# Performance work log

Measured on AMD Instinct MI355X. Metric: run time of the kernel, lower is better.

Reference implementation:

```python
import jax, jax.numpy as jnp
import numpy as np
from math import sqrt

KERNEL = 25
INV_SQRT2 = 1.0 / sqrt(2.0)


def _moving_avg(xt):
    # xt: [B, L]; replicate-pad then average-pool k=25 stride=1 -> [B, L]
    pad_l = (KERNEL - 1) // 2
    pad_r = KERNEL - 1 - pad_l
    xp = jnp.pad(xt, ((0, 0), (pad_l, pad_r)), mode='edge')[:, None, :]  # [B,1,Lp]
    k = jnp.full((1, 1, KERNEL), 1.0 / KERNEL, dtype=xt.dtype)  # [O,I,W]
    out = jax.lax.conv_general_dilated(xp, k, window_strides=(1,), padding='VALID',
                                       dimension_numbers=('NCH', 'OIH', 'NCH'))
    return out[:, 0, :]


def setup_inputs() -> dict:
    key = jax.random.key(0)
    ks = jax.random.split(key, 7)
    B, L, P, H = 8192, 4096, 720, 2048
    return {
        'x': jax.random.normal(ks[0], (B, L, 1), dtype=jnp.float32),
        'W_trend': jax.random.normal(ks[1], (P, L), dtype=jnp.float32) * 0.02,
        'b_trend': jax.random.normal(ks[2], (P,), dtype=jnp.float32) * 0.02,
        'W_lo': jax.random.normal(ks[3], (P, H), dtype=jnp.float32) * 0.02,
        'b_lo': jax.random.normal(ks[4], (P,), dtype=jnp.float32) * 0.02,
        'W_hi': jax.random.normal(ks[5], (P, H), dtype=jnp.float32) * 0.02,
        'b_hi': jax.random.normal(ks[6], (P,), dtype=jnp.float32) * 0.02,
    }


def reference(x, W_trend, b_trend, W_lo, b_lo, W_hi, b_hi):
    xt = x[..., 0]                              # [B, L]
    trend = _moving_avg(xt)                     # [B, L]
    res = xt - trend                            # [B, L]
    res_mean = jnp.mean(res, axis=-1, keepdims=True)
    # torch.std is unbiased (ddof=1)
    res_std = jnp.std(res, axis=-1, keepdims=True, ddof=1) + 1e-5
    res_norm = (res - res_mean) / res_std       # [B, L]
    # Haar DWT (stride-2 conv with [1,1]/sqrt2 and [1,-1]/sqrt2); L even -> no pad
    even, odd = res_norm[:, 0::2], res_norm[:, 1::2]  # [B, L/2]
    res_lo = (even + odd) * INV_SQRT2
    res_hi = (even - odd) * INV_SQRT2
    pred_trend = trend @ W_trend.T + b_trend    # [B, P]
    pred_res = (res_lo @ W_lo.T + b_lo) + (res_hi @ W_hi.T + b_hi)
    total = pred_trend + pred_res * res_std     # res_std broadcasts [B,1]
    return total[..., None]                     # [B, P, 1]
```

## Files before the change

kernel.cpp:

```cpp
#include <hip/hip_runtime.h>

typedef unsigned short u16;
typedef unsigned int   u32;
typedef __attribute__((ext_vector_type(8))) short bf16x8;
typedef __attribute__((ext_vector_type(4))) float f32x4;

#define LROW 4096
#define NB   8192
#define PCOL 720
#define NPAD 768
#define HH   2048
#define INV_SQRT2F 0.70710678118654752440f

#define WS_XBF_BYTES ((size_t)67108864)
#define WS_G_BYTES   ((size_t)6291456)
#define WS_MIN       (WS_XBF_BYTES + WS_G_BYTES + (size_t)NB * 4)

__device__ __forceinline__ u16 f2bf(float f) {
    union { float f; u32 u; } v; v.f = f;
    u32 r = v.u + 0x7FFFu + ((v.u >> 16) & 1u);
    return (u16)(r >> 16);
}

#define SWZ(i) ((i) ^ (((i) >> 5) & 31))

__global__ __launch_bounds__(256) void prep_rows(const float* __restrict__ x,
                                                 u16* __restrict__ xbf,
                                                 float* __restrict__ stdv) {
    __shared__ float S[LROW];
    __shared__ float wred[4];
    __shared__ float ends[2];
    __shared__ float rred[8];
    const int tid = threadIdx.x;
    const int lane = tid & 63, wv = tid >> 6;
    const size_t b = blockIdx.x;

    const float4* xr4 = (const float4*)(x + b * LROW);
    float4 q0 = xr4[tid * 4 + 0], q1 = xr4[tid * 4 + 1];
    float4 q2 = xr4[tid * 4 + 2], q3 = xr4[tid * 4 + 3];
    float r[16];
    r[0]=q0.x; r[1]=q0.y; r[2]=q0.z; r[3]=q0.w;
    r[4]=q1.x; r[5]=q1.y; r[6]=q1.z; r[7]=q1.w;
    r[8]=q2.x; r[9]=q2.y; r[10]=q2.z; r[11]=q2.w;
    r[12]=q3.x; r[13]=q3.y; r[14]=q3.z; r[15]=q3.w;

    float ps[16];
    float a = 0.f;
    #pragma unroll
    for (int k = 0; k < 16; ++k) { a += r[k]; ps[k] = a; }
    const float segsum = a;

    float v = segsum;
    #pragma unroll
    for (int off = 1; off < 64; off <<= 1) {
        float o = __shfl_up(v, off);
        if (lane >= off) v += o;
    }
    if (lane == 63) wred[wv] = v;
    if (tid == 0)   ends[0] = r[0];
    if (tid == 255) ends[1] = r[15];
    __syncthreads();

    float wbase = 0.f;
    #pragma unroll
    for (int w = 0; w < 4; ++w) if (w < wv) wbase += wred[w];
    const float ebase = wbase + v - segsum;

    #pragma unroll
    for (int k = 0; k < 16; ++k) {
        const int i = (tid << 4) + k;
        S[SWZ(i)] = ebase + ps[k];
    }
    __syncthreads();

    const float x0 = ends[0], xl = ends[1];
    float s1 = 0.f, s2 = 0.f;
    u16 ob[16];
    #pragma unroll
    for (int k = 0; k < 16; ++k) {
        const int i = (tid << 4) + k;
        int h = i + 12; h = h > LROW - 1 ? LROW - 1 : h;
        float wsum = S[SWZ(h)];
        if (i >= 13) wsum -= S[SWZ(i - 13)];
        if (i < 12) wsum += (float)(12 - i) * x0;
        if (i > LROW - 13) wsum += (float)(i - (LROW - 13)) * xl;
        const float xi = r[k];
        const float rr = xi - wsum * 0.04f;
        s1 += rr; s2 += rr * rr;
        ob[k] = f2bf(xi);
    }

    uint4 o0, o1;
    o0.x = (u32)ob[0]  | ((u32)ob[1]  << 16);
    o0.y = (u32)ob[2]  | ((u32)ob[3]  << 16);
    o0.z = (u32)ob[4]  | ((u32)ob[5]  << 16);
    o0.w = (u32)ob[6]  | ((u32)ob[7]  << 16);
    o1.x = (u32)ob[8]  | ((u32)ob[9]  << 16);
    o1.y = (u32)ob[10] | ((u32)ob[11] << 16);
    o1.z = (u32)ob[12] | ((u32)ob[13] << 16);
    o1.w = (u32)ob[14] | ((u32)ob[15] << 16);
    uint4* op = (uint4*)(xbf + b * LROW + ((size_t)tid << 4));
    op[0] = o0; op[1] = o1;

    #pragma unroll
    for (int off = 32; off; off >>= 1) {
        s1 += __shfl_down(s1, off);
        s2 += __shfl_down(s2, off);
    }
    if (lane == 0) { rred[wv * 2] = s1; rred[wv * 2 + 1] = s2; }
    __syncthreads();
    if (tid == 0) {
        const float S1 = rred[0] + rred[2] + rred[4] + rred[6];
        const float S2 = rred[1] + rred[3] + rred[5] + rred[7];
        const float mean = S1 / (float)LROW;
        float var = (S2 - (float)LROW * mean * mean) / (float)(LROW - 1);
        var = var < 0.f ? 0.f : var;
        stdv[b] = sqrtf(var) + 1e-5f;
    }
}

__global__ __launch_bounds__(256) void prep_weights(const float* __restrict__ Wt,
                                                    const float* __restrict__ Wlo,
                                                    const float* __restrict__ Whi,
                                                    u16* __restrict__ Gm) {
    __shared__ float S[LROW];
    __shared__ float wred[4];
    __shared__ float sred[4];
    const int tid = threadIdx.x;
    const int lane = tid & 63, wv = tid >> 6;
    const int p = blockIdx.x;
    u16* grow = Gm + (size_t)p * LROW;
    if (p >= PCOL) {
        uint4 z; z.x = z.y = z.z = z.w = 0u;
        uint4* g4 = (uint4*)grow;
        for (int i = tid; i < LROW / 8; i += 256) g4[i] = z;
        return;
    }
    const float4* wt4 = (const float4*)(Wt + (size_t)p * LROW);
    float4 q0 = wt4[tid * 4 + 0], q1 = wt4[tid * 4 + 1];
    float4 q2 = wt4[tid * 4 + 2], q3 = wt4[tid * 4 + 3];
    const float4* lo4 = (const float4*)(Wlo + (size_t)p * HH);
    const float4* hi4 = (const float4*)(Whi + (size_t)p * HH);
    float4 a0 = lo4[tid * 2 + 0], a1 = lo4[tid * 2 + 1];
    float4 b0 = hi4[tid * 2 + 0], b1 = hi4[tid * 2 + 1];

    float w[16];
    w[0]=q0.x; w[1]=q0.y; w[2]=q0.z; w[3]=q0.w;
    w[4]=q1.x; w[5]=q1.y; w[6]=q1.z; w[7]=q1.w;
    w[8]=q2.x; w[9]=q2.y; w[10]=q2.z; w[11]=q2.w;
    w[12]=q3.x; w[13]=q3.y; w[14]=q3.z; w[15]=q3.w;
    float lv[8] = {a0.x,a0.y,a0.z,a0.w,a1.x,a1.y,a1.z,a1.w};
    float hv[8] = {b0.x,b0.y,b0.z,b0.w,b1.x,b1.y,b1.z,b1.w};

    float u[16], z_[16];
    float slo = 0.f;
    #pragma unroll
    for (int j = 0; j < 8; ++j) {
        u[2*j]   = (lv[j] + hv[j]) * INV_SQRT2F;
        u[2*j+1] = (lv[j] - hv[j]) * INV_SQRT2F;
        slo += lv[j];
    }
    #pragma unroll
    for (int k = 0; k < 16; ++k) z_[k] = w[k] - u[k];

    float ps[16];
    float a = 0.f;
    #pragma unroll
    for (int k = 0; k < 16; ++k) { a += z_[k]; ps[k] = a; }
    const float segsum = a;

    float v = segsum;
    #pragma unroll
    for (int off = 1; off < 64; off <<= 1) {
        float o = __shfl_up(v, off);
        if (lane >= off) v += o;
    }
    if (lane == 63) wred[wv] = v;
    #pragma unroll
    for (int off = 32; off; off >>= 1) slo += __shfl_down(slo, off);
    if (lane == 0) sred[wv] = slo;
    __syncthreads();

    float wbase = 0.f;
    #pragma unroll
    for (int ww = 0; ww < 4; ++ww) if (ww < wv) wbase += wred[ww];
    const float ebase = wbase + v - segsum;
    const float SLO = sred[0] + sred[1] + sred[2] + sred[3];

    #pragma unroll
    for (int k = 0; k < 16; ++k) {
        const int i = (tid << 4) + k;
        S[SWZ(i)] = ebase + ps[k];
    }
    __syncthreads();

    const float coef = -1.4142135623730951f * SLO / (float)LROW;
    u16 ob[16];
    #pragma unroll
    for (int k = 0; k < 16; ++k) {
        const int l = (tid << 4) + k;
        float zT;
        if (l == 0) {
            float acc = 0.f;
            for (int m = 0; m <= 12; ++m) acc += S[SWZ(m)];
            zT = acc * 0.04f;
        } else if (l == LROW - 1) {
            float acc = 0.f;
            for (int m = 0; m <= 12; ++m) acc += S[SWZ(LROW - 2 - m)];
            zT = (13.f * S[SWZ(LROW - 1)] - acc) * 0.04f;
        } else {
            int h = l + 12; h = h > LROW - 1 ? LROW - 1 : h;
            float t_ = S[SWZ(h)];
            if (l >= 13) t_ -= S[SWZ(l - 13)];
            zT = t_ * 0.04f;
        }
        float c;
        const int dmin = l < (LROW - 1 - l) ? l : (LROW - 1 - l);
        if (dmin >= 12)      c = 0.f;
        else if (dmin == 0)  c = -66.f / 25.f;
        else                 c = (float)(12 - dmin) * 0.04f;
        ob[k] = f2bf(zT + u[k] + coef * c);
    }

    uint4 o0, o1;
    o0.x = (u32)ob[0]  | ((u32)ob[1]  << 16);
    o0.y = (u32)ob[2]  | ((u32)ob[3]  << 16);
    o0.z = (u32)ob[4]  | ((u32)ob[5]  << 16);
    o0.w = (u32)ob[6]  | ((u32)ob[7]  << 16);
    o1.x = (u32)ob[8]  | ((u32)ob[9]  << 16);
    o1.y = (u32)ob[10] | ((u32)ob[11] << 16);
    o1.z = (u32)ob[12] | ((u32)ob[13] << 16);
    o1.w = (u32)ob[14] | ((u32)ob[15] << 16);
    uint4* op = (uint4*)(grow + ((size_t)tid << 4));
    op[0] = o0; op[1] = o1;
}

typedef __attribute__((address_space(1))) void gvoid;
typedef __attribute__((address_space(3))) void lvoid;
__device__ __forceinline__ void gld16(const void* g, void* l) {
    __builtin_amdgcn_global_load_lds((gvoid*)g, (lvoid*)l, 16, 0, 0);
}

#define TILE_B   14336
#define NTILES   128

#define WAITVM(a, b) do { \
    if (wid < 2) asm volatile("s_waitcnt vmcnt(" #a ")" ::: "memory"); \
    else         asm volatile("s_waitcnt vmcnt(" #b ")" ::: "memory"); \
} while (0)

#define STAGE(T) do { \
    char* sb_ = smb + ((T) & 3) * TILE_B; \
    const size_t go_ = (size_t)(T) * 64; \
    gld16(g0 + go_, sb_ + lo0); \
    gld16(g1 + go_, sb_ + lo1); \
    gld16(g2 + go_, sb_ + lo2); \
    if (wid < 2) gld16(g3 + go_, sb_ + lo3); \
} while (0)

#define BODY(T, VMA, VMB, DOSTAGE) do { \
    WAITVM(VMA, VMB); \
    __builtin_amdgcn_s_barrier(); \
    __builtin_amdgcn_sched_barrier(0); \
    const char* sa_ = smb + ((T) & 3) * TILE_B; \
    bf16x8 af0 = *(const bf16x8*)(sa_ + aoff); \
    bf16x8 af1 = *(const bf16x8*)(sa_ + aoff + 1024); \
    bf16x8 af2 = *(const bf16x8*)(sa_ + aoff + 2048); \
    bf16x8 af3 = *(const bf16x8*)(sa_ + aoff + 3072); \
    bf16x8 bv0 = *(const bf16x8*)(sa_ + boff); \
    bf16x8 bv1 = *(const bf16x8*)(sa_ + boff + 1024); \
    bf16x8 bv2 = *(const bf16x8*)(sa_ + boff + 2048); \
    if (DOSTAGE) STAGE((T) + 3); \
    asm volatile("s_waitcnt lgkmcnt(0)" ::: "memory"); \
    __builtin_amdgcn_sched_barrier(0); \
    __builtin_amdgcn_s_setprio(1); \
    acc[0][0] = __builtin_amdgcn_mfma_f32_16x16x32_bf16(af0, bv0, acc[0][0], 0, 0, 0); \
    acc[0][1] = __builtin_amdgcn_mfma_f32_16x16x32_bf16(af0, bv1, acc[0][1], 0, 0, 0); \
    acc[0][2] = __builtin_amdgcn_mfma_f32_16x16x32_bf16(af0, bv2, acc[0][2], 0, 0, 0); \
    acc[1][0] = __builtin_amdgcn_mfma_f32_16x16x32_bf16(af1, bv0, acc[1][0], 0, 0, 0); \
    acc[1][1] = __builtin_amdgcn_mfma_f32_16x16x32_bf16(af1, bv1, acc[1][1], 0, 0, 0); \
    acc[1][2] = __builtin_amdgcn_mfma_f32_16x16x32_bf16(af1, bv2, acc[1][2], 0, 0, 0); \
    acc[2][0] = __builtin_amdgcn_mfma_f32_16x16x32_bf16(af2, bv0, acc[2][0], 0, 0, 0); \
    acc[2][1] = __builtin_amdgcn_mfma_f32_16x16x32_bf16(af2, bv1, acc[2][1], 0, 0, 0); \
    acc[2][2] = __builtin_amdgcn_mfma_f32_16x16x32_bf16(af2, bv2, acc[2][2], 0, 0, 0); \
    acc[3][0] = __builtin_amdgcn_mfma_f32_16x16x32_bf16(af3, bv0, acc[3][0], 0, 0, 0); \
    acc[3][1] = __builtin_amdgcn_mfma_f32_16x16x32_bf16(af3, bv1, acc[3][1], 0, 0, 0); \
    acc[3][2] = __builtin_amdgcn_mfma_f32_16x16x32_bf16(af3, bv2, acc[3][2], 0, 0, 0); \
    __builtin_amdgcn_s_setprio(0); \
} while (0)

__global__ __launch_bounds__(256, 2) void gemm_fused(const u16* __restrict__ Abf,
                                                     const u16* __restrict__ Gbf,
                                                     const float* __restrict__ bt,
                                                     const float* __restrict__ bl,
                                                     const float* __restrict__ bh,
                                                     const float* __restrict__ stdv,
                                                     float* __restrict__ out) {
    __shared__ __align__(16) char Sm[4 * TILE_B];
    char* smb = (char*)Sm;
    const int tid = threadIdx.x;
    const int l = tid & 63, wid = tid >> 6;

    const int orig = blockIdx.x;
    const int chunk = orig & 7, pos = orig >> 3;
    const int bx = pos & 7;
    const int by = (chunk << 3) + (pos >> 3);
    const int m0 = by * 128;
    const int n0 = bx * 96;

    const int sgb = (((l & 3) ^ ((l >> 3) & 3)) << 4);
    const int rsub = l >> 2;
    const char* gmat = (wid < 2) ? (const char*)Abf : (const char*)Gbf;
    const int row00 = (wid < 2) ? (m0 + wid * 64) : (n0 + (wid - 2) * 48);
    const int lob   = (wid < 2) ? (wid * 4096) : (8192 + (wid - 2) * 3072);
    const char* g0 = gmat + (((size_t)(row00 +  0 + rsub)) << 13) + sgb;
    const char* g1 = gmat + (((size_t)(row00 + 16 + rsub)) << 13) + sgb;
    const char* g2 = gmat + (((size_t)(row00 + 32 + rsub)) << 13) + sgb;
    const char* g3 = gmat + (((size_t)(row00 + 48 + rsub)) << 13) + sgb;
    const int lo0 = lob, lo1 = lob + 1024, lo2 = lob + 2048, lo3 = lob + 3072;

    const int wm = wid >> 1, wn = wid & 1;
    const int soff = (((l >> 4) ^ ((l >> 1) & 3)) << 4);
    const int aoff = (wm * 64 + (l & 15)) * 64 + soff;
    const int boff = 8192 + (wn * 48 + (l & 15)) * 64 + soff;

    f32x4 acc[4][3] = {};

    STAGE(0); STAGE(1); STAGE(2);

    for (int t = 0; t < NTILES - 3; ++t) {
        BODY(t, 8, 6, 1);
    }
    BODY(NTILES - 3, 8, 6, 0);
    BODY(NTILES - 2, 4, 3, 0);
    BODY(NTILES - 1, 0, 0, 0);

    const int crow = m0 + wm * 64 + ((l >> 4) << 2);
    const int ccol = n0 + wn * 48 + (l & 15);
    float btv[3], bsv[3];
    #pragma unroll
    for (int n = 0; n < 3; ++n) {
        const int col = ccol + n * 16;
        if (col < PCOL) { btv[n] = bt[col]; bsv[n] = bl[col] + bh[col]; }
        else            { btv[n] = 0.f; bsv[n] = 0.f; }
    }
    #pragma unroll
    for (int m = 0; m < 4; ++m) {
        const int row = crow + m * 16;
        const float4 sv = *(const float4*)(stdv + row);
        #pragma unroll
        for (int n = 0; n < 3; ++n) {
            const int col = ccol + n * 16;
            if (col < PCOL) {
                float* orow = out + (size_t)row * PCOL + col;
                #pragma unroll
                for (int j = 0; j < 4; ++j) {
                    const float s = (j == 0) ? sv.x : (j == 1) ? sv.y : (j == 2) ? sv.z : sv.w;
                    orow[(size_t)j * PCOL] = acc[m][n][j] + btv[n] + s * bsv[n];
                }
            }
        }
    }
}

extern "C" void kernel_launch(void* const* d_in, const int* in_sizes, int n_in,
                              void* d_out, int out_size, void* d_ws, size_t ws_size,
                              hipStream_t stream) {
    (void)in_sizes; (void)n_in; (void)out_size;
    if (ws_size < WS_MIN) return;

    const float* x  = (const float*)d_in[0];
    const float* Wt = (const float*)d_in[1];
    const float* bt = (const float*)d_in[2];
    const float* Wl = (const float*)d_in[3];
    const float* bl = (const float*)d_in[4];
    const float* Wh = (const float*)d_in[5];
    const float* bh = (const float*)d_in[6];
    float* out = (float*)d_out;

    char* ws = (char*)d_ws;
    u16*   xbf = (u16*)ws;
    u16*   Gm  = (u16*)(ws + WS_XBF_BYTES);
    float* sd  = (float*)(ws + WS_XBF_BYTES + WS_G_BYTES);

    prep_rows<<<NB, 256, 0, stream>>>(x, xbf, sd);
    prep_weights<<<NPAD, 256, 0, stream>>>(Wt, Wl, Wh, Gm);
    gemm_fused<<<512, 256, 0, stream>>>(xbf, Gm, bt, bl, bh, sd, out);
}
```

Baseline: 112.9 us.

## Load A fragments directly to registers, stage only B through LDS with K=64 tiles

The GEMM main loop no longer stages the A operand through shared memory. Each wave loads its A fragments straight from global memory into double-buffered registers one tile ahead. Only the weight (B) tile goes through a 3-buffer LDS ring via global_load_lds, and the K tile doubles to 64 so each barrier covers 24 MFMAs instead of 12. This cuts LDS traffic and barrier count, at the cost of more VGPRs, uncoalesced-style direct global loads for A, and a single vmcnt(8) wait that assumes a particular instruction ordering.

```diff
diff --git a/kernel.cpp b/kernel.cpp
--- a/kernel.cpp
+++ b/kernel.cpp
@@ -237,55 +237,69 @@
 
 typedef __attribute__((address_space(1))) void gvoid;
 typedef __attribute__((address_space(3))) void lvoid;
-__device__ __forceinline__ void gld16(const void* g, void* l) {
-    __builtin_amdgcn_global_load_lds((gvoid*)g, (lvoid*)l, 16, 0, 0);
-}
-
-#define TILE_B   14336
-#define NTILES   128
-
-#define WAITVM(a, b) do { \
-    if (wid < 2) asm volatile("s_waitcnt vmcnt(" #a ")" ::: "memory"); \
-    else         asm volatile("s_waitcnt vmcnt(" #b ")" ::: "memory"); \
+#define GLD16(g, l_) __builtin_amdgcn_global_load_lds((gvoid*)(g), (lvoid*)(l_), 16, 0, 0)
+#define MF(a, b, c) __builtin_amdgcn_mfma_f32_16x16x32_bf16(a, b, c, 0, 0, 0)
+
+#define BBUF 12288
+
+#define STAGE_B(T, STOFF) do { \
+    const size_t go_ = (size_t)(T) * 128; \
+    GLD16(gb0 + go_, Sm + (STOFF) + lb0); \
+    GLD16(gb1 + go_, Sm + (STOFF) + lb1); \
+    GLD16(gb2 + go_, Sm + (STOFF) + lb2); \
 } while (0)
 
-#define STAGE(T) do { \
-    char* sb_ = smb + ((T) & 3) * TILE_B; \
-    const size_t go_ = (size_t)(T) * 64; \
-    gld16(g0 + go_, sb_ + lo0); \
-    gld16(g1 + go_, sb_ + lo1); \
-    gld16(g2 + go_, sb_ + lo2); \
-    if (wid < 2) gld16(g3 + go_, sb_ + lo3); \
+#define LOAD_A(T, S) do { \
+    const char* s_ = pa + (size_t)(T) * 128; \
+    S[0][0] = *(const bf16x8*)(s_); \
+    S[0][1] = *(const bf16x8*)(s_ + 131072); \
+    S[0][2] = *(const bf16x8*)(s_ + 262144); \
+    S[0][3] = *(const bf16x8*)(s_ + 393216); \
+    S[1][0] = *(const bf16x8*)(s_ + 64); \
+    S[1][1] = *(const bf16x8*)(s_ + 131072 + 64); \
+    S[1][2] = *(const bf16x8*)(s_ + 262144 + 64); \
+    S[1][3] = *(const bf16x8*)(s_ + 393216 + 64); \
 } while (0)
 
-#define BODY(T, VMA, VMB, DOSTAGE) do { \
-    WAITVM(VMA, VMB); \
+#define ITER(T, AC, AL, RDOFF, STOFF, DOSTAGE, DOLOADA) do { \
+    asm volatile("s_waitcnt vmcnt(8) lgkmcnt(0)" ::: "memory"); \
     __builtin_amdgcn_s_barrier(); \
     __builtin_amdgcn_sched_barrier(0); \
-    const char* sa_ = smb + ((T) & 3) * TILE_B; \
-    bf16x8 af0 = *(const bf16x8*)(sa_ + aoff); \
-    bf16x8 af1 = *(const bf16x8*)(sa_ + aoff + 1024); \
-    bf16x8 af2 = *(const bf16x8*)(sa_ + aoff + 2048); \
-    bf16x8 af3 = *(const bf16x8*)(sa_ + aoff + 3072); \
-    bf16x8 bv0 = *(const bf16x8*)(sa_ + boff); \
-    bf16x8 bv1 = *(const bf16x8*)(sa_ + boff + 1024); \
-    bf16x8 bv2 = *(const bf16x8*)(sa_ + boff + 2048); \
-    if (DOSTAGE) STAGE((T) + 3); \
-    asm volatile("s_waitcnt lgkmcnt(0)" ::: "memory"); \
+    if (DOSTAGE) { STAGE_B((T) + 2, STOFF); } \
     __builtin_amdgcn_sched_barrier(0); \
+    if (DOLOADA) { LOAD_A((T) + 1, AL); } \
+    const char* r_ = (const char*)Sm + (RDOFF); \
+    bf16x8 b00 = *(const bf16x8*)(r_ + lofs0); \
+    bf16x8 b01 = *(const bf16x8*)(r_ + lofs0 + 2048); \
+    bf16x8 b02 = *(const bf16x8*)(r_ + lofs0 + 4096); \
+    bf16x8 b10 = *(const bf16x8*)(r_ + lofs1); \
+    bf16x8 b11 = *(const bf16x8*)(r_ + lofs1 + 2048); \
+    bf16x8 b12 = *(const bf16x8*)(r_ + lofs1 + 4096); \
     __builtin_amdgcn_s_setprio(1); \
-    acc[0][0] = __builtin_amdgcn_mfma_f32_16x16x32_bf16(af0, bv0, acc[0][0], 0, 0, 0); \
-    acc[0][1] = __builtin_amdgcn_mfma_f32_16x16x32_bf16(af0, bv1, acc[0][1], 0, 0, 0); \
-    acc[0][2] = __builtin_amdgcn_mfma_f32_16x16x32_bf16(af0, bv2, acc[0][2], 0, 0, 0); \
-    acc[1][0] = __builtin_amdgcn_mfma_f32_16x16x32_bf16(af1, bv0, acc[1][0], 0, 0, 0); \
-    acc[1][1] = __builtin_amdgcn_mfma_f32_16x16x32_bf16(af1, bv1, acc[1][1], 0, 0, 0); \
-    acc[1][2] = __builtin_amdgcn_mfma_f32_16x16x32_bf16(af1, bv2, acc[1][2], 0, 0, 0); \
-    acc[2][0] = __builtin_amdgcn_mfma_f32_16x16x32_bf16(af2, bv0, acc[2][0], 0, 0, 0); \
-    acc[2][1] = __builtin_amdgcn_mfma_f32_16x16x32_bf16(af2, bv1, acc[2][1], 0, 0, 0); \
-    acc[2][2] = __builtin_amdgcn_mfma_f32_16x16x32_bf16(af2, bv2, acc[2][2], 0, 0, 0); \
-    acc[3][0] = __builtin_amdgcn_mfma_f32_16x16x32_bf16(af3, bv0, acc[3][0], 0, 0, 0); \
-    acc[3][1] = __builtin_amdgcn_mfma_f32_16x16x32_bf16(af3, bv1, acc[3][1], 0, 0, 0); \
-    acc[3][2] = __builtin_amdgcn_mfma_f32_16x16x32_bf16(af3, bv2, acc[3][2], 0, 0, 0); \
+    acc[0][0] = MF(AC[0][0], b00, acc[0][0]); \
+    acc[0][1] = MF(AC[0][0], b01, acc[0][1]); \
+    acc[0][2] = MF(AC[0][0], b02, acc[0][2]); \
+    acc[1][0] = MF(AC[0][1], b00, acc[1][0]); \
+    acc[1][1] = MF(AC[0][1], b01, acc[1][1]); \
+    acc[1][2] = MF(AC[0][1], b02, acc[1][2]); \
+    acc[2][0] = MF(AC[0][2], b00, acc[2][0]); \
+    acc[2][1] = MF(AC[0][2], b01, acc[2][1]); \
+    acc[2][2] = MF(AC[0][2], b02, acc[2][2]); \
+    acc[3][0] = MF(AC[0][3], b00, acc[3][0]); \
+    acc[3][1] = MF(AC[0][3], b01, acc[3][1]); \
+    acc[3][2] = MF(AC[0][3], b02, acc[3][2]); \
+    acc[0][0] = MF(AC[1][0], b10, acc[0][0]); \
+    acc[0][1] = MF(AC[1][0], b11, acc[0][1]); \
+    acc[0][2] = MF(AC[1][0], b12, acc[0][2]); \
+    acc[1][0] = MF(AC[1][1], b10, acc[1][0]); \
+    acc[1][1] = MF(AC[1][1], b11, acc[1][1]); \
+    acc[1][2] = MF(AC[1][1], b12, acc[1][2]); \
+    acc[2][0] = MF(AC[1][2], b10, acc[2][0]); \
+    acc[2][1] = MF(AC[1][2], b11, acc[2][1]); \
+    acc[2][2] = MF(AC[1][2], b12, acc[2][2]); \
+    acc[3][0] = MF(AC[1][3], b10, acc[3][0]); \
+    acc[3][1] = MF(AC[1][3], b11, acc[3][1]); \
+    acc[3][2] = MF(AC[1][3], b12, acc[3][2]); \
     __builtin_amdgcn_s_setprio(0); \
 } while (0)
 
@@ -296,10 +310,10 @@
                                                      const float* __restrict__ bh,
                                                      const float* __restrict__ stdv,
                                                      float* __restrict__ out) {
-    __shared__ __align__(16) char Sm[4 * TILE_B];
-    char* smb = (char*)Sm;
+    __shared__ __align__(16) char Sm[3 * BBUF];
     const int tid = threadIdx.x;
     const int l = tid & 63, wid = tid >> 6;
+    const int wm = wid >> 1, wn = wid & 1;
 
     const int orig = blockIdx.x;
     const int chunk = orig & 7, pos = orig >> 3;
@@ -308,32 +322,40 @@
     const int m0 = by * 128;
     const int n0 = bx * 96;
 
-    const int sgb = (((l & 3) ^ ((l >> 3) & 3)) << 4);
-    const int rsub = l >> 2;
-    const char* gmat = (wid < 2) ? (const char*)Abf : (const char*)Gbf;
-    const int row00 = (wid < 2) ? (m0 + wid * 64) : (n0 + (wid - 2) * 48);
-    const int lob   = (wid < 2) ? (wid * 4096) : (8192 + (wid - 2) * 3072);
-    const char* g0 = gmat + (((size_t)(row00 +  0 + rsub)) << 13) + sgb;
-    const char* g1 = gmat + (((size_t)(row00 + 16 + rsub)) << 13) + sgb;
-    const char* g2 = gmat + (((size_t)(row00 + 32 + rsub)) << 13) + sgb;
-    const char* g3 = gmat + (((size_t)(row00 + 48 + rsub)) << 13) + sgb;
-    const int lo0 = lob, lo1 = lob + 1024, lo2 = lob + 2048, lo3 = lob + 3072;
-
-    const int wm = wid >> 1, wn = wid & 1;
-    const int soff = (((l >> 4) ^ ((l >> 1) & 3)) << 4);
-    const int aoff = (wm * 64 + (l & 15)) * 64 + soff;
-    const int boff = 8192 + (wn * 48 + (l & 15)) * 64 + soff;
+    const char* pa = (const char*)Abf
+        + ((size_t)(m0 + wm * 64 + (l & 15)) << 13) + ((l >> 4) << 4);
+
+    const int sgb = (((l & 7) ^ (l >> 3)) << 4);
+    const char* gb0 = (const char*)Gbf + ((size_t)(n0 + wid * 24 +  0 + (l >> 3)) << 13) + sgb;
+    const char* gb1 = (const char*)Gbf + ((size_t)(n0 + wid * 24 +  8 + (l >> 3)) << 13) + sgb;
+    const char* gb2 = (const char*)Gbf + ((size_t)(n0 + wid * 24 + 16 + (l >> 3)) << 13) + sgb;
+    const int lb0 = (wid * 3 + 0) * 1024;
+    const int lb1 = (wid * 3 + 1) * 1024;
+    const int lb2 = (wid * 3 + 2) * 1024;
+
+    const int lofs0 = (wn * 48 + (l & 15)) * 128 + ((((l >> 4)    ) ^ (l & 7)) << 4);
+    const int lofs1 = (wn * 48 + (l & 15)) * 128 + ((((l >> 4) + 4) ^ (l & 7)) << 4);
 
     f32x4 acc[4][3] = {};
-
-    STAGE(0); STAGE(1); STAGE(2);
-
-    for (int t = 0; t < NTILES - 3; ++t) {
-        BODY(t, 8, 6, 1);
-    }
-    BODY(NTILES - 3, 8, 6, 0);
-    BODY(NTILES - 2, 4, 3, 0);
-    BODY(NTILES - 1, 0, 0, 0);
+    bf16x8 A0F[2][4], A1F[2][4];
+
+    STAGE_B(0, 0);
+    STAGE_B(1, BBUF);
+    __builtin_amdgcn_sched_barrier(0);
+    LOAD_A(0, A0F);
+
+    for (int t = 0; t < 60; t += 6) {
+        ITER(t + 0, A0F, A1F, 0,        2 * BBUF, 1, 1);
+        ITER(t + 1, A1F, A0F, BBUF,     0,        1, 1);
+        ITER(t + 2, A0F, A1F, 2 * BBUF, BBUF,     1, 1);
+        ITER(t + 3, A1F, A0F, 0,        2 * BBUF, 1, 1);
+        ITER(t + 4, A0F, A1F, BBUF,     0,        1, 1);
+        ITER(t + 5, A1F, A0F, 2 * BBUF, BBUF,     1, 1);
+    }
+    ITER(60, A0F, A1F, 0,        2 * BBUF, 1, 1);
+    ITER(61, A1F, A0F, BBUF,     0,        1, 1);
+    ITER(62, A0F, A1F, 2 * BBUF, 0,        0, 1);
+    ITER(63, A1F, A0F, 0,        0,        0, 0);
 
     const int crow = m0 + wm * 64 + ((l >> 4) << 2);
     const int ccol = n0 + wn * 48 + (l & 15);
```

Result: slower. 177.1 us (+56.8%).

## Split GEMM K across wave pairs with 512-thread blocks and staggered A/B staging

Applied to the files above, without the earlier changes.

The GEMM kernel now runs 8 waves per block instead of 4. Wave pairs split each 128-wide K tile in half, and the partial accumulators are reduced through shared memory in the epilogue. A and B staging is split into separate triple- and double-buffered rings with different prefetch distances, using 128-byte K tiles and a new swizzle. The aim is more latency hiding and MFMA issue parallelism per CU, at the cost of an extra LDS reduction, more LDS per block, and fewer blocks resident at once.

```diff
diff --git a/kernel.cpp b/kernel.cpp
--- a/kernel.cpp
+++ b/kernel.cpp
@@ -237,69 +237,65 @@
 
 typedef __attribute__((address_space(1))) void gvoid;
 typedef __attribute__((address_space(3))) void lvoid;
-__device__ __forceinline__ void gld16(const void* g, void* l) {
-    __builtin_amdgcn_global_load_lds((gvoid*)g, (lvoid*)l, 16, 0, 0);
-}
-
-#define TILE_B   14336
-#define NTILES   128
-
-#define WAITVM(a, b) do { \
-    if (wid < 2) asm volatile("s_waitcnt vmcnt(" #a ")" ::: "memory"); \
-    else         asm volatile("s_waitcnt vmcnt(" #b ")" ::: "memory"); \
+#define GLD16(g, l_) __builtin_amdgcn_global_load_lds((gvoid*)(g), (lvoid*)(l_), 16, 0, 0)
+#define MF(a, b, c) __builtin_amdgcn_mfma_f32_16x16x32_bf16(a, b, c, 0, 0, 0)
+
+#define ABUF 16384
+#define BBASE 49152
+#define BBUF 12288
+
+#define STAGE_A2(T, DB) do { \
+    char* d_ = Sm + (DB) * ABUF; \
+    const size_t go_ = (size_t)((T) + 2) * 128; \
+    GLD16(s0 + go_, d_ + dof0); GLD16(s1 + go_, d_ + dof1); \
+    GLD16(s2 + go_, d_ + dof2); GLD16(s3 + go_, d_ + dof3); \
 } while (0)
 
-#define STAGE(T) do { \
-    char* sb_ = smb + ((T) & 3) * TILE_B; \
-    const size_t go_ = (size_t)(T) * 64; \
-    gld16(g0 + go_, sb_ + lo0); \
-    gld16(g1 + go_, sb_ + lo1); \
-    gld16(g2 + go_, sb_ + lo2); \
-    if (wid < 2) gld16(g3 + go_, sb_ + lo3); \
+#define STAGE_B1(T, DB) do { \
+    char* d_ = Sm + BBASE + (DB) * BBUF; \
+    const size_t go_ = (size_t)((T) + 1) * 128; \
+    GLD16(s0 + go_, d_ + dof0); GLD16(s1 + go_, d_ + dof1); GLD16(s2 + go_, d_ + dof2); \
 } while (0)
 
-#define BODY(T, VMA, VMB, DOSTAGE) do { \
-    WAITVM(VMA, VMB); \
+#define ITER(T, RA, RB, SAB, SBB, VA, VB, SA, SB) do { \
+    if (isA) { asm volatile("s_waitcnt vmcnt(" #VA ")" ::: "memory"); } \
+    else     { asm volatile("s_waitcnt vmcnt(" #VB ")" ::: "memory"); } \
     __builtin_amdgcn_s_barrier(); \
     __builtin_amdgcn_sched_barrier(0); \
-    const char* sa_ = smb + ((T) & 3) * TILE_B; \
-    bf16x8 af0 = *(const bf16x8*)(sa_ + aoff); \
-    bf16x8 af1 = *(const bf16x8*)(sa_ + aoff + 1024); \
-    bf16x8 af2 = *(const bf16x8*)(sa_ + aoff + 2048); \
-    bf16x8 af3 = *(const bf16x8*)(sa_ + aoff + 3072); \
-    bf16x8 bv0 = *(const bf16x8*)(sa_ + boff); \
-    bf16x8 bv1 = *(const bf16x8*)(sa_ + boff + 1024); \
-    bf16x8 bv2 = *(const bf16x8*)(sa_ + boff + 2048); \
-    if (DOSTAGE) STAGE((T) + 3); \
+    if (isA) { if (SA) STAGE_A2(T, SAB); } \
+    else     { if (SB) STAGE_B1(T, SBB); } \
+    __builtin_amdgcn_sched_barrier(0); \
+    const char* ab_ = Sm + (RA) * ABUF + aro; \
+    const char* bb_ = Sm + BBASE + (RB) * BBUF + bro; \
+    bf16x8 a0_ = *(const bf16x8*)(ab_); \
+    bf16x8 a1_ = *(const bf16x8*)(ab_ + 2048); \
+    bf16x8 a2_ = *(const bf16x8*)(ab_ + 4096); \
+    bf16x8 a3_ = *(const bf16x8*)(ab_ + 6144); \
+    bf16x8 b0_ = *(const bf16x8*)(bb_); \
+    bf16x8 b1_ = *(const bf16x8*)(bb_ + 2048); \
+    bf16x8 b2_ = *(const bf16x8*)(bb_ + 4096); \
     asm volatile("s_waitcnt lgkmcnt(0)" ::: "memory"); \
     __builtin_amdgcn_sched_barrier(0); \
     __builtin_amdgcn_s_setprio(1); \
-    acc[0][0] = __builtin_amdgcn_mfma_f32_16x16x32_bf16(af0, bv0, acc[0][0], 0, 0, 0); \
-    acc[0][1] = __builtin_amdgcn_mfma_f32_16x16x32_bf16(af0, bv1, acc[0][1], 0, 0, 0); \
-    acc[0][2] = __builtin_amdgcn_mfma_f32_16x16x32_bf16(af0, bv2, acc[0][2], 0, 0, 0); \
-    acc[1][0] = __builtin_amdgcn_mfma_f32_16x16x32_bf16(af1, bv0, acc[1][0], 0, 0, 0); \
-    acc[1][1] = __builtin_amdgcn_mfma_f32_16x16x32_bf16(af1, bv1, acc[1][1], 0, 0, 0); \
-    acc[1][2] = __builtin_amdgcn_mfma_f32_16x16x32_bf16(af1, bv2, acc[1][2], 0, 0, 0); \
-    acc[2][0] = __builtin_amdgcn_mfma_f32_16x16x32_bf16(af2, bv0, acc[2][0], 0, 0, 0); \
-    acc[2][1] = __builtin_amdgcn_mfma_f32_16x16x32_bf16(af2, bv1, acc[2][1], 0, 0, 0); \
-    acc[2][2] = __builtin_amdgcn_mfma_f32_16x16x32_bf16(af2, bv2, acc[2][2], 0, 0, 0); \
-    acc[3][0] = __builtin_amdgcn_mfma_f32_16x16x32_bf16(af3, bv0, acc[3][0], 0, 0, 0); \
-    acc[3][1] = __builtin_amdgcn_mfma_f32_16x16x32_bf16(af3, bv1, acc[3][1], 0, 0, 0); \
-    acc[3][2] = __builtin_amdgcn_mfma_f32_16x16x32_bf16(af3, bv2, acc[3][2], 0, 0, 0); \
+    acc[0][0]=MF(a0_,b0_,acc[0][0]); acc[0][1]=MF(a0_,b1_,acc[0][1]); acc[0][2]=MF(a0_,b2_,acc[0][2]); \
+    acc[1][0]=MF(a1_,b0_,acc[1][0]); acc[1][1]=MF(a1_,b1_,acc[1][1]); acc[1][2]=MF(a1_,b2_,acc[1][2]); \
+    acc[2][0]=MF(a2_,b0_,acc[2][0]); acc[2][1]=MF(a2_,b1_,acc[2][1]); acc[2][2]=MF(a2_,b2_,acc[2][2]); \
+    acc[3][0]=MF(a3_,b0_,acc[3][0]); acc[3][1]=MF(a3_,b1_,acc[3][1]); acc[3][2]=MF(a3_,b2_,acc[3][2]); \
     __builtin_amdgcn_s_setprio(0); \
 } while (0)
 
-__global__ __launch_bounds__(256, 2) void gemm_fused(const u16* __restrict__ Abf,
+__global__ __launch_bounds__(512, 4) void gemm_fused(const u16* __restrict__ Abf,
                                                      const u16* __restrict__ Gbf,
                                                      const float* __restrict__ bt,
                                                      const float* __restrict__ bl,
                                                      const float* __restrict__ bh,
                                                      const float* __restrict__ stdv,
                                                      float* __restrict__ out) {
-    __shared__ __align__(16) char Sm[4 * TILE_B];
-    char* smb = (char*)Sm;
+    __shared__ __align__(16) char Sm[73728];
     const int tid = threadIdx.x;
     const int l = tid & 63, wid = tid >> 6;
+    const int kp = wid & 1, wm = (wid >> 1) & 1, wn = wid >> 2;
+    const bool isA = (wid < 4);
 
     const int orig = blockIdx.x;
     const int chunk = orig & 7, pos = orig >> 3;
@@ -308,55 +304,92 @@
     const int m0 = by * 128;
     const int n0 = bx * 96;
 
-    const int sgb = (((l & 3) ^ ((l >> 3) & 3)) << 4);
-    const int rsub = l >> 2;
-    const char* gmat = (wid < 2) ? (const char*)Abf : (const char*)Gbf;
-    const int row00 = (wid < 2) ? (m0 + wid * 64) : (n0 + (wid - 2) * 48);
-    const int lob   = (wid < 2) ? (wid * 4096) : (8192 + (wid - 2) * 3072);
-    const char* g0 = gmat + (((size_t)(row00 +  0 + rsub)) << 13) + sgb;
-    const char* g1 = gmat + (((size_t)(row00 + 16 + rsub)) << 13) + sgb;
-    const char* g2 = gmat + (((size_t)(row00 + 32 + rsub)) << 13) + sgb;
-    const char* g3 = gmat + (((size_t)(row00 + 48 + rsub)) << 13) + sgb;
-    const int lo0 = lob, lo1 = lob + 1024, lo2 = lob + 2048, lo3 = lob + 3072;
-
-    const int wm = wid >> 1, wn = wid & 1;
-    const int soff = (((l >> 4) ^ ((l >> 1) & 3)) << 4);
-    const int aoff = (wm * 64 + (l & 15)) * 64 + soff;
-    const int boff = 8192 + (wn * 48 + (l & 15)) * 64 + soff;
+    const int sgb = (((l & 7) ^ (l >> 3)) << 4);
+    const char* s0; const char* s1; const char* s2; const char* s3;
+    int dof0, dof1, dof2, dof3;
+    if (isA) {
+        const int r0 = wid * 32;
+        s0 = (const char*)Abf + ((size_t)(m0 + r0 +  0 + (l >> 3)) << 13) + sgb;
+        s1 = (const char*)Abf + ((size_t)(m0 + r0 +  8 + (l >> 3)) << 13) + sgb;
+        s2 = (const char*)Abf + ((size_t)(m0 + r0 + 16 + (l >> 3)) << 13) + sgb;
+        s3 = (const char*)Abf + ((size_t)(m0 + r0 + 24 + (l >> 3)) << 13) + sgb;
+        dof0 = r0 * 128; dof1 = dof0 + 1024; dof2 = dof0 + 2048; dof3 = dof0 + 3072;
+    } else {
+        const int r0 = (wid - 4) * 24;
+        s0 = (const char*)Gbf + ((size_t)(n0 + r0 +  0 + (l >> 3)) << 13) + sgb;
+        s1 = (const char*)Gbf + ((size_t)(n0 + r0 +  8 + (l >> 3)) << 13) + sgb;
+        s2 = (const char*)Gbf + ((size_t)(n0 + r0 + 16 + (l >> 3)) << 13) + sgb;
+        s3 = s0;
+        dof0 = r0 * 128; dof1 = dof0 + 1024; dof2 = dof0 + 2048; dof3 = dof0;
+    }
+
+    const int slot = ((kp << 2) + (l >> 4)) ^ (l & 7);
+    const int aro = (wm * 64 + (l & 15)) * 128 + (slot << 4);
+    const int bro = (wn * 48 + (l & 15)) * 128 + (slot << 4);
 
     f32x4 acc[4][3] = {};
 
-    STAGE(0); STAGE(1); STAGE(2);
-
-    for (int t = 0; t < NTILES - 3; ++t) {
-        BODY(t, 8, 6, 1);
-    }
-    BODY(NTILES - 3, 8, 6, 0);
-    BODY(NTILES - 2, 4, 3, 0);
-    BODY(NTILES - 1, 0, 0, 0);
-
-    const int crow = m0 + wm * 64 + ((l >> 4) << 2);
-    const int ccol = n0 + wn * 48 + (l & 15);
-    float btv[3], bsv[3];
-    #pragma unroll
-    for (int n = 0; n < 3; ++n) {
-        const int col = ccol + n * 16;
-        if (col < PCOL) { btv[n] = bt[col]; bsv[n] = bl[col] + bh[col]; }
-        else            { btv[n] = 0.f; bsv[n] = 0.f; }
-    }
-    #pragma unroll
-    for (int m = 0; m < 4; ++m) {
-        const int row = crow + m * 16;
-        const float4 sv = *(const float4*)(stdv + row);
+    if (isA) {
+        GLD16(s0, Sm + dof0); GLD16(s1, Sm + dof1);
+        GLD16(s2, Sm + dof2); GLD16(s3, Sm + dof3);
+        GLD16(s0 + 128, Sm + ABUF + dof0); GLD16(s1 + 128, Sm + ABUF + dof1);
+        GLD16(s2 + 128, Sm + ABUF + dof2); GLD16(s3 + 128, Sm + ABUF + dof3);
+    } else {
+        GLD16(s0, Sm + BBASE + dof0); GLD16(s1, Sm + BBASE + dof1);
+        GLD16(s2, Sm + BBASE + dof2);
+    }
+
+    for (int t = 0; t < 60; t += 6) {
+        ITER(t + 0, 0, 0, 2, 1, 4, 0, 1, 1);
+        ITER(t + 1, 1, 1, 0, 0, 4, 0, 1, 1);
+        ITER(t + 2, 2, 0, 1, 1, 4, 0, 1, 1);
+        ITER(t + 3, 0, 1, 2, 0, 4, 0, 1, 1);
+        ITER(t + 4, 1, 0, 0, 1, 4, 0, 1, 1);
+        ITER(t + 5, 2, 1, 1, 0, 4, 0, 1, 1);
+    }
+    ITER(60, 0, 0, 2, 1, 4, 0, 1, 1);
+    ITER(61, 1, 1, 0, 0, 4, 0, 1, 1);
+    ITER(62, 2, 0, 1, 1, 4, 0, 0, 1);
+    ITER(63, 0, 1, 2, 0, 0, 0, 0, 0);
+
+    __syncthreads();
+    float* red = (float*)Sm;
+    const int pb_ = (wm * 2 + wn) * 3264;
+    const int rr_ = (l >> 4) << 2;
+    const int cc_ = l & 15;
+    if (kp == 1) {
+        #pragma unroll
+        for (int m = 0; m < 4; ++m)
+            #pragma unroll
+            for (int n = 0; n < 3; ++n)
+                *(f32x4*)(red + pb_ + (n * 16 + cc_) * 68 + m * 16 + rr_) = acc[m][n];
+    }
+    __syncthreads();
+    if (kp == 0) {
+        const int crow = m0 + wm * 64 + rr_;
+        const int ccol = n0 + wn * 48 + cc_;
+        float btv[3], bsv[3];
         #pragma unroll
         for (int n = 0; n < 3; ++n) {
             const int col = ccol + n * 16;
-            if (col < PCOL) {
-                float* orow = out + (size_t)row * PCOL + col;
-                #pragma unroll
-                for (int j = 0; j < 4; ++j) {
-                    const float s = (j == 0) ? sv.x : (j == 1) ? sv.y : (j == 2) ? sv.z : sv.w;
-                    orow[(size_t)j * PCOL] = acc[m][n][j] + btv[n] + s * bsv[n];
+            if (col < PCOL) { btv[n] = bt[col]; bsv[n] = bl[col] + bh[col]; }
+            else            { btv[n] = 0.f; bsv[n] = 0.f; }
+        }
+        #pragma unroll
+        for (int m = 0; m < 4; ++m) {
+            const int row = crow + m * 16;
+            const float4 sv = *(const float4*)(stdv + row);
+            #pragma unroll
+            for (int n = 0; n < 3; ++n) {
+                const int col = ccol + n * 16;
+                if (col < PCOL) {
+                    const f32x4 pv = *(const f32x4*)(red + pb_ + (n * 16 + cc_) * 68 + m * 16 + rr_);
+                    float* orow = out + (size_t)row * PCOL + col;
+                    #pragma unroll
+                    for (int j = 0; j < 4; ++j) {
+                        const float s = (j == 0) ? sv.x : (j == 1) ? sv.y : (j == 2) ? sv.z : sv.w;
+                        orow[(size_t)j * PCOL] = acc[m][n][j] + pv[j] + btv[n] + s * bsv[n];
+                    }
                 }
             }
         }
@@ -385,5 +418,5 @@
 
     prep_rows<<<NB, 256, 0, stream>>>(x, xbf, sd);
     prep_weights<<<NPAD, 256, 0, stream>>>(Wt, Wl, Wh, Gm);
-    gemm_fused<<<512, 256, 0, stream>>>(xbf, Gm, bt, bl, bh, sd, out);
+    gemm_fused<<<512, 512, 0, stream>>>(xbf, Gm, bt, bl, bh, sd, out);
 }
```

Result: faster. 100.2 us (-11.2%).
